# Optimization experiments

Hardware: AMD Instinct MI355X
Metric: run time of the kernel (lower is better)

The kernel has to match this reference:

```python
import jax, jax.numpy as jnp
import numpy as np

# Assumptions from DCalhas/eeg_to_fmri repo layers:
#  - RandomFourierFeatures: z = cos(x @ W + b) followed by layer normalization
#    over the feature axis (normalization='layer'), W/b trainable.
#  - Sinusoids: elementwise sin(x).

B, D, T, L = 64, 512, 1024, 512

def _layer_norm(x, eps=1e-5):
    mu = jnp.mean(x, axis=-1, keepdims=True)
    var = jnp.var(x, axis=-1, keepdims=True)
    return (x - mu) * jax.lax.rsqrt(var + eps)

def setup_inputs() -> dict:
    key = jax.random.key(0)
    ks = jax.random.split(key, 12)
    s = 1.0 / np.sqrt(L)
    return {
        "x": jax.random.normal(ks[0], (B, D, T), jnp.float32),
        "rff_w": jax.random.normal(ks[1], (D, L), jnp.float32) * (1.0 / np.sqrt(D)),
        "rff_b": jax.random.uniform(ks[2], (L,), jnp.float32, 0.0, 2.0 * np.pi),
        "weight_input": jax.random.normal(ks[3], (L, L), jnp.float32) * s,
        "weight_forget": jax.random.normal(ks[4], (L, L), jnp.float32) * s,
        "weight_context": jax.random.normal(ks[5], (L, L), jnp.float32) * s,
        "recurrent_input": jax.random.normal(ks[6], (L, L), jnp.float32) * s,
        "recurrent_forget": jax.random.normal(ks[7], (L, L), jnp.float32) * s,
        "recurrent_context": jax.random.normal(ks[8], (L, L), jnp.float32) * s,
        "bias_input": jnp.zeros((L,), jnp.float32),
        "bias_forget": jnp.zeros((L,), jnp.float32),
        "bias_context": jnp.zeros((L,), jnp.float32),
        "init_latent": jax.random.normal(ks[9], (1, 1, L), jnp.float32) * s,
        "init_context": jax.random.normal(ks[10], (1, 1, L), jnp.float32) * s,
    }

def reference(x, rff_w, rff_b, weight_input, weight_forget, weight_context,
              recurrent_input, recurrent_forget, recurrent_context,
              bias_input, bias_forget, bias_context, init_latent, init_context):
    b = x.shape[0]
    xt = jnp.transpose(x, (0, 2, 1))                      # [B,T,D]
    z = _layer_norm(jnp.cos(xt @ rff_w + rff_b))          # [B,T,L]
    # hidden_states[t+1] = z_t in the original loop, so the "recurrent" input
    # at step t is z_{t-1} (init_latent at t=0). Gates are thus batchable.
    z_prev = jnp.concatenate(
        [jnp.broadcast_to(init_latent, (b, 1, z.shape[2])), z[:, :-1]], axis=1)
    i = jax.nn.sigmoid(z @ weight_input + z_prev @ recurrent_input + bias_input)
    f = jax.nn.sigmoid(z @ weight_forget + z_prev @ recurrent_forget + bias_forget)
    g = jnp.tanh(z @ weight_context + z_prev @ recurrent_context + bias_context)
    o = jnp.sin(z)                                        # Sinusoids gate

    c0 = jnp.broadcast_to(init_context[:, 0], (b, z.shape[2]))  # [B,L]
    def step(c_prev, gates):
        i_t, f_t, g_t, o_t = gates
        c_t = f_t * c_prev + i_t * g_t
        return c_t, o_t * c_t
    xs = tuple(jnp.transpose(a, (1, 0, 2)) for a in (i, f, g, o))  # time-major
    _, h = jax.lax.scan(step, c0, xs)                     # [T,B,L]
    return jnp.transpose(h, (1, 2, 0))                    # [B,L,T]
```

## Files before the change

kernel.cpp:

```cpp
#include <hip/hip_runtime.h>
#include <hip/hip_bf16.h>
#include <hip/hip_fp16.h>
#include <cstdint>
#include <cstddef>


typedef float f32x4 __attribute__((ext_vector_type(4)));
typedef short s16x8 __attribute__((ext_vector_type(8)));

__device__ __forceinline__ void gload_lds16(const void* g, void* l) {
  __builtin_amdgcn_global_load_lds(
      (const __attribute__((address_space(1))) void*)g,
      (__attribute__((address_space(3))) void*)l, 16, 0, 0);
}
__device__ __forceinline__ ushort f2bf(float f) {
  uint32_t u = __float_as_uint(f);
  return (ushort)((u + 0x7FFF + ((u >> 16) & 1)) >> 16);
}
__device__ __forceinline__ float bf2f(ushort s) {
  return __uint_as_float(((uint32_t)s) << 16);
}
__device__ __forceinline__ ushort f2h(float f) {
  return __half_as_ushort(__float2half(f));
}
__device__ __forceinline__ float h2f(ushort s) {
  return __half2float(__ushort_as_half(s));
}

#define MF(d, a, b) d = __builtin_amdgcn_mfma_f32_16x16x32_bf16(a, b, d, 0, 0, 0);

__global__ __launch_bounds__(256) void transpose_cvt(
    const float* __restrict__ src, ushort* __restrict__ dst, int ld)
{
  __shared__ float tile[32][33];
  const int c0 = blockIdx.x * 32, r0 = blockIdx.y * 32;
  const int tx = threadIdx.x & 31, ty = threadIdx.x >> 5;
#pragma unroll
  for (int i = 0; i < 4; ++i)
    tile[ty + i * 8][tx] = src[(size_t)(r0 + ty + i * 8) * 512 + c0 + tx];
  __syncthreads();
#pragma unroll
  for (int i = 0; i < 4; ++i)
    dst[(size_t)(c0 + ty + i * 8) * ld + r0 + tx] = f2bf(tile[tx][ty + i * 8]);
}

__global__ __launch_bounds__(256) void transpose6(
    const float* __restrict__ s0, const float* __restrict__ s1,
    const float* __restrict__ s2, const float* __restrict__ s3,
    const float* __restrict__ s4, const float* __restrict__ s5,
    const float* __restrict__ il, ushort* __restrict__ W2t,
    ushort* __restrict__ ilb)
{
  const int z = blockIdx.z;
  if (z == 6) {
    if (blockIdx.x == 0 && blockIdx.y == 0) {
      ilb[threadIdx.x] = f2bf(il[threadIdx.x]);
      ilb[threadIdx.x + 256] = f2bf(il[threadIdx.x + 256]);
    }
    return;
  }
  const float* src = z == 0 ? s0 : z == 1 ? s1 : z == 2 ? s2
                   : z == 3 ? s3 : z == 4 ? s4 : s5;
  ushort* dst = W2t + (size_t)(z >> 1) * 512 * 1024 + (z & 1) * 512;
  __shared__ float tile[32][33];
  const int c0 = blockIdx.x * 32, r0 = blockIdx.y * 32;
  const int tx = threadIdx.x & 31, ty = threadIdx.x >> 5;
#pragma unroll
  for (int i = 0; i < 4; ++i)
    tile[ty + i * 8][tx] = src[(size_t)(r0 + ty + i * 8) * 512 + c0 + tx];
  __syncthreads();
#pragma unroll
  for (int i = 0; i < 4; ++i)
    dst[(size_t)(c0 + ty + i * 8) * 1024 + r0 + tx] = f2bf(tile[tx][ty + i * 8]);
}

__global__ __launch_bounds__(256) void transpose_x(
    const float* __restrict__ x, ushort* __restrict__ xt)
{
  __shared__ float tile[64][68];
  const int b = blockIdx.z;
  const int t0 = blockIdx.x * 64, d0 = blockIdx.y * 64;
  const float* src = x + ((size_t)b * 512 + d0) * 1024 + t0;
  const int lr_ = threadIdx.x >> 4, lc4 = (threadIdx.x & 15) * 4;
#pragma unroll
  for (int p = 0; p < 4; ++p) {
    const float4 v = *(const float4*)(src + (size_t)(lr_ + p * 16) * 1024 + lc4);
    *(float4*)&tile[lr_ + p * 16][lc4] = v;
  }
  __syncthreads();
  const int tt = threadIdx.x >> 2, dc = (threadIdx.x & 3) * 16;
  ushort* dst = xt + ((size_t)b * 1024 + t0 + tt) * 512 + d0 + dc;
  uint4 o1, o2;
  o1.x = (uint)f2bf(tile[dc + 0][tt]) | ((uint)f2bf(tile[dc + 1][tt]) << 16);
  o1.y = (uint)f2bf(tile[dc + 2][tt]) | ((uint)f2bf(tile[dc + 3][tt]) << 16);
  o1.z = (uint)f2bf(tile[dc + 4][tt]) | ((uint)f2bf(tile[dc + 5][tt]) << 16);
  o1.w = (uint)f2bf(tile[dc + 6][tt]) | ((uint)f2bf(tile[dc + 7][tt]) << 16);
  o2.x = (uint)f2bf(tile[dc + 8][tt]) | ((uint)f2bf(tile[dc + 9][tt]) << 16);
  o2.y = (uint)f2bf(tile[dc + 10][tt]) | ((uint)f2bf(tile[dc + 11][tt]) << 16);
  o2.z = (uint)f2bf(tile[dc + 12][tt]) | ((uint)f2bf(tile[dc + 13][tt]) << 16);
  o2.w = (uint)f2bf(tile[dc + 14][tt]) | ((uint)f2bf(tile[dc + 15][tt]) << 16);
  *(uint4*)(dst) = o1;
  *(uint4*)(dst + 8) = o2;
}

__global__ __launch_bounds__(256, 2) void k1_mfma(
    const ushort* __restrict__ A, const ushort* __restrict__ Bt,
    const float* __restrict__ bias, ushort* __restrict__ U)
{
  __shared__ __align__(16) short As[128 * 64];
  __shared__ __align__(16) short Bs[128 * 64];
  const int tid = threadIdx.x;
  const int lane = tid & 63, wid = tid >> 6;
  const int orig = blockIdx.x;
  const int swz = (orig & 7) * 256 + (orig >> 3);
  const int n0 = (swz & 3) * 128, r0 = (swz >> 2) * 128;
  const int wr = wid >> 1, wc = wid & 1;
  const int fr = lane & 15, fq = lane >> 4;
  const int lr = lane >> 3;
  const int swz_el = ((lane & 7) ^ lr) * 8;

  const int RA = r0 + wid * 32 + lr;
  const ushort* pa0 = A + (size_t)(RA)      * 512 + swz_el;
  const ushort* pa1 = A + (size_t)(RA + 8)  * 512 + swz_el;
  const ushort* pa2 = A + (size_t)(RA + 16) * 512 + swz_el;
  const ushort* pa3 = A + (size_t)(RA + 24) * 512 + swz_el;
  const int RB = n0 + wid * 32 + lr;
  const ushort* pb0 = Bt + (size_t)(RB)      * 512 + swz_el;
  const ushort* pb1 = Bt + (size_t)(RB + 8)  * 512 + swz_el;
  const ushort* pb2 = Bt + (size_t)(RB + 16) * 512 + swz_el;
  const ushort* pb3 = Bt + (size_t)(RB + 24) * 512 + swz_el;
  char* dA = (char*)As + wid * 4096;
  char* dB = (char*)Bs + wid * 4096;

  const int so0 = fr * 64 + ((fq)     ^ (fr & 7)) * 8;
  const int so1 = fr * 64 + ((4 + fq) ^ (fr & 7)) * 8;

  f32x4 c00 = {0.f,0.f,0.f,0.f}, c01 = c00, c02 = c00, c03 = c00,
        c10 = c00, c11 = c00, c12 = c00, c13 = c00,
        c20 = c00, c21 = c00, c22 = c00, c23 = c00,
        c30 = c00, c31 = c00, c32 = c00, c33 = c00;

  for (int k0 = 0; k0 < 512; k0 += 64) {
    gload_lds16(pa0 + k0, dA);        gload_lds16(pa1 + k0, dA + 1024);
    gload_lds16(pa2 + k0, dA + 2048); gload_lds16(pa3 + k0, dA + 3072);
    gload_lds16(pb0 + k0, dB);        gload_lds16(pb1 + k0, dB + 1024);
    gload_lds16(pb2 + k0, dB + 2048); gload_lds16(pb3 + k0, dB + 3072);
    __syncthreads();
    const s16x8 a00 = *(const s16x8*)&As[wr * 4096 + 0 * 1024 + so0];
    const s16x8 a01 = *(const s16x8*)&As[wr * 4096 + 0 * 1024 + so1];
    const s16x8 a10 = *(const s16x8*)&As[wr * 4096 + 1 * 1024 + so0];
    const s16x8 a11 = *(const s16x8*)&As[wr * 4096 + 1 * 1024 + so1];
    const s16x8 a20 = *(const s16x8*)&As[wr * 4096 + 2 * 1024 + so0];
    const s16x8 a21 = *(const s16x8*)&As[wr * 4096 + 2 * 1024 + so1];
    const s16x8 a30 = *(const s16x8*)&As[wr * 4096 + 3 * 1024 + so0];
    const s16x8 a31 = *(const s16x8*)&As[wr * 4096 + 3 * 1024 + so1];
    const s16x8 b00 = *(const s16x8*)&Bs[wc * 4096 + 0 * 1024 + so0];
    const s16x8 b01 = *(const s16x8*)&Bs[wc * 4096 + 0 * 1024 + so1];
    const s16x8 b10 = *(const s16x8*)&Bs[wc * 4096 + 1 * 1024 + so0];
    const s16x8 b11 = *(const s16x8*)&Bs[wc * 4096 + 1 * 1024 + so1];
    const s16x8 b20 = *(const s16x8*)&Bs[wc * 4096 + 2 * 1024 + so0];
    const s16x8 b21 = *(const s16x8*)&Bs[wc * 4096 + 2 * 1024 + so1];
    const s16x8 b30 = *(const s16x8*)&Bs[wc * 4096 + 3 * 1024 + so0];
    const s16x8 b31 = *(const s16x8*)&Bs[wc * 4096 + 3 * 1024 + so1];
    MF(c00, a00, b00) MF(c01, a00, b10) MF(c02, a00, b20) MF(c03, a00, b30)
    MF(c10, a10, b00) MF(c11, a10, b10) MF(c12, a10, b20) MF(c13, a10, b30)
    MF(c20, a20, b00) MF(c21, a20, b10) MF(c22, a20, b20) MF(c23, a20, b30)
    MF(c30, a30, b00) MF(c31, a30, b10) MF(c32, a30, b20) MF(c33, a30, b30)
    MF(c00, a01, b01) MF(c01, a01, b11) MF(c02, a01, b21) MF(c03, a01, b31)
    MF(c10, a11, b01) MF(c11, a11, b11) MF(c12, a11, b21) MF(c13, a11, b31)
    MF(c20, a21, b01) MF(c21, a21, b11) MF(c22, a21, b21) MF(c23, a21, b31)
    MF(c30, a31, b01) MF(c31, a31, b11) MF(c32, a31, b21) MF(c33, a31, b31)
    __syncthreads();
  }

#define EPI1(cmn, m_, n_) { \
    const int col = n0 + wc * 64 + n_ * 16 + fr; \
    const float bv = bias[col]; \
    const int rbase = r0 + wr * 64 + m_ * 16 + fq * 4; \
    _Pragma("unroll") for (int j = 0; j < 4; ++j) \
      U[(size_t)(rbase + j) * 512 + col] = f2bf(cosf(cmn[j] + bv)); }
  EPI1(c00, 0, 0) EPI1(c01, 0, 1) EPI1(c02, 0, 2) EPI1(c03, 0, 3)
  EPI1(c10, 1, 0) EPI1(c11, 1, 1) EPI1(c12, 1, 2) EPI1(c13, 1, 3)
  EPI1(c20, 2, 0) EPI1(c21, 2, 1) EPI1(c22, 2, 2) EPI1(c23, 2, 3)
  EPI1(c30, 3, 0) EPI1(c31, 3, 1) EPI1(c32, 3, 2) EPI1(c33, 3, 3)
#undef EPI1
}

__global__ __launch_bounds__(256) void ln_rows(
    const ushort* __restrict__ U, ushort* __restrict__ Z)
{
  const int row = blockIdx.x * 4 + (threadIdx.x >> 6);
  const int lane = threadIdx.x & 63;
  const size_t base = (size_t)row * 512 + lane * 8;
  const uint4 pk = *(const uint4*)(U + base);
  float v[8];
  v[0] = bf2f(pk.x & 0xffff); v[1] = bf2f(pk.x >> 16);
  v[2] = bf2f(pk.y & 0xffff); v[3] = bf2f(pk.y >> 16);
  v[4] = bf2f(pk.z & 0xffff); v[5] = bf2f(pk.z >> 16);
  v[6] = bf2f(pk.w & 0xffff); v[7] = bf2f(pk.w >> 16);
  float s = 0.f, s2 = 0.f;
#pragma unroll
  for (int j = 0; j < 8; ++j) { s += v[j]; s2 += v[j] * v[j]; }
#pragma unroll
  for (int m = 1; m < 64; m <<= 1) { s += __shfl_xor(s, m); s2 += __shfl_xor(s2, m); }
  const float mean = s * (1.f / 512.f);
  const float var = s2 * (1.f / 512.f) - mean * mean;
  const float inv = rsqrtf(var + 1e-5f);
  uint4 o;
  o.x = (uint)f2bf((v[0] - mean) * inv) | ((uint)f2bf((v[1] - mean) * inv) << 16);
  o.y = (uint)f2bf((v[2] - mean) * inv) | ((uint)f2bf((v[3] - mean) * inv) << 16);
  o.z = (uint)f2bf((v[4] - mean) * inv) | ((uint)f2bf((v[5] - mean) * inv) << 16);
  o.w = (uint)f2bf((v[6] - mean) * inv) | ((uint)f2bf((v[7] - mean) * inv) << 16);
  *(uint4*)(Z + base) = o;
}

__global__ __launch_bounds__(256, 2) void k2_mfma(
    const ushort* __restrict__ Z, const ushort* __restrict__ Wt,
    const ushort* __restrict__ IL,
    const float* __restrict__ biv, const float* __restrict__ bfv,
    const float* __restrict__ bcv,
    ushort* __restrict__ G2, int tc, int Tc, int nwg)
{
  __shared__ __align__(16) short As[128 * 64];
  __shared__ __align__(16) short Bs0[128 * 64];
  __shared__ __align__(16) short Bs1[128 * 64];
  const int tid = threadIdx.x;
  const int lane = tid & 63, wid = tid >> 6;
  const int cpx = nwg >> 3;
  const int orig = blockIdx.x;
  const int swz = (orig & 7) * cpx + (orig >> 3);
  const int bx = swz & 7, by = swz >> 3;
  const int nb = Tc >> 7;
  const int b = by / nb, tb = by % nb;
  const int r0g = b * 1024 + tc + tb * 128;
  const int r0c = b * Tc + tb * 128;
  const bool isig = bx < 4;
  const int n0 = (bx & 3) * 128;
  const int wr = wid >> 1, wc = wid & 1;
  const int fr = lane & 15, fq = lane >> 4;
  const int lr = lane >> 3;
  const int swz_el = ((lane & 7) ^ lr) * 8;

  const int R0 = r0g + wid * 32 + lr;
  const ushort* pa0 = Z + (size_t)(R0)      * 512 + swz_el;
  const ushort* pa1 = Z + (size_t)(R0 + 8)  * 512 + swz_el;
  const ushort* pa2 = Z + (size_t)(R0 + 16) * 512 + swz_el;
  const ushort* pa3 = Z + (size_t)(R0 + 24) * 512 + swz_el;
  const ushort* ph0 = ((((R0)      & 1023) == 0) ? IL : (Z + (size_t)(R0 - 1)  * 512)) + swz_el;
  const ushort* ph1 = ((((R0 + 8)  & 1023) == 0) ? IL : (Z + (size_t)(R0 + 7)  * 512)) + swz_el;
  const ushort* ph2 = ((((R0 + 16) & 1023) == 0) ? IL : (Z + (size_t)(R0 + 15) * 512)) + swz_el;
  const ushort* ph3 = ((((R0 + 24) & 1023) == 0) ? IL : (Z + (size_t)(R0 + 23) * 512)) + swz_el;
  const int RB0 = (isig ? n0 : 512 + n0) + wid * 32 + lr;
  const ushort* pb0 = Wt + (size_t)(RB0)      * 1024 + swz_el;
  const ushort* pb1 = Wt + (size_t)(RB0 + 8)  * 1024 + swz_el;
  const ushort* pb2 = Wt + (size_t)(RB0 + 16) * 1024 + swz_el;
  const ushort* pb3 = Wt + (size_t)(RB0 + 24) * 1024 + swz_el;
  const int RB1 = 1024 + n0 + wid * 32 + lr;
  const ushort* pq0 = Wt + (size_t)(RB1)      * 1024 + swz_el;
  const ushort* pq1 = Wt + (size_t)(RB1 + 8)  * 1024 + swz_el;
  const ushort* pq2 = Wt + (size_t)(RB1 + 16) * 1024 + swz_el;
  const ushort* pq3 = Wt + (size_t)(RB1 + 24) * 1024 + swz_el;

  const int so0 = fr * 64 + ((fq)     ^ (fr & 7)) * 8;
  const int so1 = fr * 64 + ((4 + fq) ^ (fr & 7)) * 8;

  f32x4 zz = {0.f,0.f,0.f,0.f};
  f32x4 c00=zz,c01=zz,c02=zz,c03=zz, c10=zz,c11=zz,c12=zz,c13=zz,
        c20=zz,c21=zz,c22=zz,c23=zz, c30=zz,c31=zz,c32=zz,c33=zz;
  f32x4 d00=zz,d01=zz,d02=zz,d03=zz, d10=zz,d11=zz,d12=zz,d13=zz,
        d20=zz,d21=zz,d22=zz,d23=zz, d30=zz,d31=zz,d32=zz,d33=zz;

#define STG8(P0,P1,P2,P3, KO, DST) { \
    char* d_ = (char*)(DST) + wid * 4096; \
    gload_lds16((P0) + (KO), d_);        gload_lds16((P1) + (KO), d_ + 1024); \
    gload_lds16((P2) + (KO), d_ + 2048); gload_lds16((P3) + (KO), d_ + 3072); }

#define RDA(SO) \
    const s16x8 fa0 = *(const s16x8*)&As[wr * 4096 + 0 * 1024 + (SO)]; \
    const s16x8 fa1 = *(const s16x8*)&As[wr * 4096 + 1 * 1024 + (SO)]; \
    const s16x8 fa2 = *(const s16x8*)&As[wr * 4096 + 2 * 1024 + (SO)]; \
    const s16x8 fa3 = *(const s16x8*)&As[wr * 4096 + 3 * 1024 + (SO)];

#define RDB(BS, SO) \
    const s16x8 fb0 = *(const s16x8*)&(BS)[wc * 4096 + 0 * 1024 + (SO)]; \
    const s16x8 fb1 = *(const s16x8*)&(BS)[wc * 4096 + 1 * 1024 + (SO)]; \
    const s16x8 fb2 = *(const s16x8*)&(BS)[wc * 4096 + 2 * 1024 + (SO)]; \
    const s16x8 fb3 = *(const s16x8*)&(BS)[wc * 4096 + 3 * 1024 + (SO)];

#define MMC \
    MF(c00,fa0,fb0) MF(c01,fa0,fb1) MF(c02,fa0,fb2) MF(c03,fa0,fb3) \
    MF(c10,fa1,fb0) MF(c11,fa1,fb1) MF(c12,fa1,fb2) MF(c13,fa1,fb3) \
    MF(c20,fa2,fb0) MF(c21,fa2,fb1) MF(c22,fa2,fb2) MF(c23,fa2,fb3) \
    MF(c30,fa3,fb0) MF(c31,fa3,fb1) MF(c32,fa3,fb2) MF(c33,fa3,fb3)

#define MMD \
    MF(d00,fa0,fb0) MF(d01,fa0,fb1) MF(d02,fa0,fb2) MF(d03,fa0,fb3) \
    MF(d10,fa1,fb0) MF(d11,fa1,fb1) MF(d12,fa1,fb2) MF(d13,fa1,fb3) \
    MF(d20,fa2,fb0) MF(d21,fa2,fb1) MF(d22,fa2,fb2) MF(d23,fa2,fb3) \
    MF(d30,fa3,fb0) MF(d31,fa3,fb1) MF(d32,fa3,fb2) MF(d33,fa3,fb3)

#define KSTEP(SO_) { \
    RDA(SO_) \
    { RDB(Bs0, SO_) MMC } \
    if (isig) { RDB(Bs1, SO_) MMD } }

  for (int k0 = 0; k0 < 512; k0 += 64) {
    STG8(pa0, pa1, pa2, pa3, k0, As)
    STG8(pb0, pb1, pb2, pb3, k0, Bs0)
    if (isig) { STG8(pq0, pq1, pq2, pq3, k0, Bs1) }
    __syncthreads();
    KSTEP(so0)
    KSTEP(so1)
    __syncthreads();
  }
  for (int k0 = 0; k0 < 512; k0 += 64) {
    STG8(ph0, ph1, ph2, ph3, k0, As)
    STG8(pb0, pb1, pb2, pb3, 512 + k0, Bs0)
    if (isig) { STG8(pq0, pq1, pq2, pq3, 512 + k0, Bs1) }
    __syncthreads();
    KSTEP(so0)
    KSTEP(so1)
    __syncthreads();
  }
#undef KSTEP
#undef MMD
#undef MMC
#undef RDB
#undef RDA
#undef STG8

  if (isig) {
#define EPI(cmn, dmn, m_, n_) { \
    const int col = n0 + wc * 64 + n_ * 16 + fr; \
    const float bvi = biv[col], bvc = bcv[col]; \
    const int rbase = wr * 64 + m_ * 16 + fq * 4; \
    _Pragma("unroll") for (int j = 0; j < 4; ++j) { \
      const float iv = 1.f / (1.f + __expf(-(cmn[j] + bvi))); \
      const float gv = 2.f / (1.f + __expf(-2.f * (dmn[j] + bvc))) - 1.f; \
      G2[(size_t)(r0c + rbase + j) * 1024 + col] = f2h(iv * gv); } }
    EPI(c00, d00, 0, 0) EPI(c01, d01, 0, 1) EPI(c02, d02, 0, 2) EPI(c03, d03, 0, 3)
    EPI(c10, d10, 1, 0) EPI(c11, d11, 1, 1) EPI(c12, d12, 1, 2) EPI(c13, d13, 1, 3)
    EPI(c20, d20, 2, 0) EPI(c21, d21, 2, 1) EPI(c22, d22, 2, 2) EPI(c23, d23, 2, 3)
    EPI(c30, d30, 3, 0) EPI(c31, d31, 3, 1) EPI(c32, d32, 3, 2) EPI(c33, d33, 3, 3)
#undef EPI
  } else {
#define EPI(cmn, m_, n_) { \
    const int col = n0 + wc * 64 + n_ * 16 + fr; \
    const float bv = bfv[col]; \
    const int rbase = wr * 64 + m_ * 16 + fq * 4; \
    _Pragma("unroll") for (int j = 0; j < 4; ++j) { \
      const float fv = 1.f / (1.f + __expf(-(cmn[j] + bv))); \
      G2[(size_t)(r0c + rbase + j) * 1024 + 512 + col] = f2h(fv); } }
    EPI(c00, 0, 0) EPI(c01, 0, 1) EPI(c02, 0, 2) EPI(c03, 0, 3)
    EPI(c10, 1, 0) EPI(c11, 1, 1) EPI(c12, 1, 2) EPI(c13, 1, 3)
    EPI(c20, 2, 0) EPI(c21, 2, 1) EPI(c22, 2, 2) EPI(c23, 2, 3)
    EPI(c30, 3, 0) EPI(c31, 3, 1) EPI(c32, 3, 2) EPI(c33, 3, 3)
#undef EPI
  }
}

__global__ __launch_bounds__(256) void k3a_seg(
    const ushort* __restrict__ G2, float* __restrict__ Aseg,
    float* __restrict__ Bseg, int Tc)
{
  const int l = blockIdx.x * 256 + threadIdx.x;
  const int b = blockIdx.y, s = blockIdx.z;
  const int SEGc = Tc >> 6;
  const ushort* gb = G2 + ((size_t)(b * Tc + s * 64)) * 1024 + l;
  float A = 1.f, c = 0.f;
#pragma unroll 8
  for (int j = 0; j < 64; ++j) {
    const float P = h2f(gb[(size_t)j * 1024]);
    const float F = h2f(gb[(size_t)j * 1024 + 512]);
    A *= F;
    c = fmaf(F, c, P);
  }
  const size_t o = (size_t)(b * SEGc + s) * 512 + l;
  Aseg[o] = A;
  Bseg[o] = c;
}

__global__ __launch_bounds__(512) void k3b_comb(
    const float* __restrict__ Aseg, const float* __restrict__ Bseg,
    const float* __restrict__ initc, float* __restrict__ cstart,
    float* __restrict__ cbuf, int tc, int Tc)
{
  const int b = blockIdx.x, l = threadIdx.x;
  const int SEGc = Tc >> 6;
  float c = (tc == 0) ? initc[l] : cbuf[b * 512 + l];
  for (int s = 0; s < SEGc; ++s) {
    const size_t o = (size_t)(b * SEGc + s) * 512 + l;
    cstart[o] = c;
    c = fmaf(Aseg[o], c, Bseg[o]);
  }
  cbuf[b * 512 + l] = c;
}

__global__ __launch_bounds__(128) void k3c_emit(
    const ushort* __restrict__ G2, const ushort* __restrict__ Z,
    const float* __restrict__ cstart, float* __restrict__ out,
    int tc, int Tc)
{
  __shared__ float tile[128][65];
  const int tid = threadIdx.x;
  const int l0 = blockIdx.x * 128;
  const int b = blockIdx.y, s = blockIdx.z;
  const int SEGc = Tc >> 6;
  const int l = l0 + tid;

  float c = cstart[(size_t)(b * SEGc + s) * 512 + l];
  const ushort* gb = G2 + ((size_t)(b * Tc + s * 64)) * 1024 + l;
  const ushort* zb = Z + ((size_t)(b * 1024 + tc + s * 64)) * 512 + l;
#pragma unroll 8
  for (int j = 0; j < 64; ++j) {
    const float P = h2f(gb[(size_t)j * 1024]);
    const float F = h2f(gb[(size_t)j * 1024 + 512]);
    const float zv = bf2f(zb[(size_t)j * 512]);
    c = fmaf(F, c, P);
    tile[tid][j] = sinf(zv) * c;
  }
  __syncthreads();
  const int col = tid & 63, rhalf = tid >> 6;
  const size_t obase = ((size_t)b * 512 + l0) * 1024 + (size_t)(tc + s * 64) + col;
#pragma unroll
  for (int p = 0; p < 64; ++p) {
    const int row = rhalf + p * 2;
    out[obase + (size_t)row * 1024] = tile[row][col];
  }
}

extern "C" void kernel_launch(void* const* d_in, const int* in_sizes, int n_in,
                              void* d_out, int out_size, void* d_ws, size_t ws_size,
                              hipStream_t stream)
{
  const float* x  = (const float*)d_in[0];
  const float* W  = (const float*)d_in[1];
  const float* rb = (const float*)d_in[2];
  const float* wi = (const float*)d_in[3];
  const float* wf = (const float*)d_in[4];
  const float* wc = (const float*)d_in[5];
  const float* ri = (const float*)d_in[6];
  const float* rf = (const float*)d_in[7];
  const float* rc = (const float*)d_in[8];
  const float* bi = (const float*)d_in[9];
  const float* bfo = (const float*)d_in[10];
  const float* bc = (const float*)d_in[11];
  const float* il = (const float*)d_in[12];
  const float* ic = (const float*)d_in[13];
  float* out = (float*)d_out;

  char* ws = (char*)d_ws;
  size_t off = 0;
  auto alloc = [&](size_t bytes) -> void* {
    void* p = ws + off;
    off = (off + bytes + 255) & ~(size_t)255;
    return p;
  };
  ushort* z    = (ushort*)alloc((size_t)65536 * 512 * 2);
  ushort* W1t  = (ushort*)alloc((size_t)512 * 512 * 2);
  ushort* W2t  = (ushort*)alloc((size_t)1536 * 1024 * 2);
  ushort* ilb  = (ushort*)alloc(512 * 2);
  float*  cbuf = (float*)alloc((size_t)64 * 512 * 4);
  float*  Aseg = (float*)alloc((size_t)64 * 16 * 512 * 4);
  float*  Bseg = (float*)alloc((size_t)64 * 16 * 512 * 4);
  float*  cstart = (float*)alloc((size_t)64 * 16 * 512 * 4);
  const size_t fixed_end = off;
  ushort* xt   = (ushort*)alloc((size_t)65536 * 512 * 2);
  ushort* G2   = (ushort*)(ws + fixed_end);
  ushort* u    = (ushort*)d_out;

  int Tc = 1024;
  while (Tc > 128 && fixed_end + (size_t)64 * Tc * 1024 * 2 > ws_size) Tc >>= 1;

  transpose_cvt<<<dim3(16, 16), 256, 0, stream>>>(W, W1t, 512);
  transpose6<<<dim3(16, 16, 7), 256, 0, stream>>>(wi, ri, wf, rf, wc, rc, il, W2t, ilb);
  transpose_x<<<dim3(16, 8, 64), 256, 0, stream>>>(x, xt);

  k1_mfma<<<dim3(2048), 256, 0, stream>>>(xt, W1t, rb, u);
  ln_rows<<<16384, 256, 0, stream>>>(u, z);

  for (int tc = 0; tc < 1024; tc += Tc) {
    const int SEGc = Tc >> 6;
    const int nwg2 = 8 * 64 * (Tc >> 7);
    k2_mfma<<<dim3(nwg2), 256, 0, stream>>>(
        z, W2t, ilb, bi, bfo, bc, G2, tc, Tc, nwg2);
    k3a_seg<<<dim3(2, 64, SEGc), 256, 0, stream>>>(G2, Aseg, Bseg, Tc);
    k3b_comb<<<64, 512, 0, stream>>>(Aseg, Bseg, ic, cstart, cbuf, tc, Tc);
    k3c_emit<<<dim3(4, 64, SEGc), 128, 0, stream>>>(G2, z, cstart, out, tc, Tc);
  }
}
```

Measured before the change: 568.1 us.

## Balance k2 workgroups so forget-gate blocks compute two column tiles each

k2 previously launched 8 column groups per row tile. The 4 input/context blocks each ran two accumulator sets, while the 4 forget blocks ran only one and sat half idle. Now there are 6 groups, and each forget block computes 256 columns using both accumulator sets, so all workgroups do equal work and the grid is smaller. The W1 transpose is also folded into the combined weight-transpose kernel, removing one launch. The swizzle now uses mod/div by 6 instead of bit ops, and fewer workgroups may lower occupancy or tail balance.

```diff
diff --git a/kernel.cpp b/kernel.cpp
--- a/kernel.cpp
+++ b/kernel.cpp
@@ -29,27 +29,13 @@
 
 #define MF(d, a, b) d = __builtin_amdgcn_mfma_f32_16x16x32_bf16(a, b, d, 0, 0, 0);
 
-__global__ __launch_bounds__(256) void transpose_cvt(
-    const float* __restrict__ src, ushort* __restrict__ dst, int ld)
-{
-  __shared__ float tile[32][33];
-  const int c0 = blockIdx.x * 32, r0 = blockIdx.y * 32;
-  const int tx = threadIdx.x & 31, ty = threadIdx.x >> 5;
-#pragma unroll
-  for (int i = 0; i < 4; ++i)
-    tile[ty + i * 8][tx] = src[(size_t)(r0 + ty + i * 8) * 512 + c0 + tx];
-  __syncthreads();
-#pragma unroll
-  for (int i = 0; i < 4; ++i)
-    dst[(size_t)(c0 + ty + i * 8) * ld + r0 + tx] = f2bf(tile[tx][ty + i * 8]);
-}
-
-__global__ __launch_bounds__(256) void transpose6(
+__global__ __launch_bounds__(256) void transpose8(
     const float* __restrict__ s0, const float* __restrict__ s1,
     const float* __restrict__ s2, const float* __restrict__ s3,
     const float* __restrict__ s4, const float* __restrict__ s5,
-    const float* __restrict__ il, ushort* __restrict__ W2t,
-    ushort* __restrict__ ilb)
+    const float* __restrict__ il, const float* __restrict__ W1,
+    ushort* __restrict__ W2t, ushort* __restrict__ ilb,
+    ushort* __restrict__ W1t)
 {
   const int z = blockIdx.z;
   if (z == 6) {
@@ -60,8 +46,10 @@
     return;
   }
   const float* src = z == 0 ? s0 : z == 1 ? s1 : z == 2 ? s2
-                   : z == 3 ? s3 : z == 4 ? s4 : s5;
-  ushort* dst = W2t + (size_t)(z >> 1) * 512 * 1024 + (z & 1) * 512;
+                   : z == 3 ? s3 : z == 4 ? s4 : z == 5 ? s5 : W1;
+  ushort* dst = (z == 7) ? W1t
+              : W2t + (size_t)(z >> 1) * 512 * 1024 + (z & 1) * 512;
+  const int ld = (z == 7) ? 512 : 1024;
   __shared__ float tile[32][33];
   const int c0 = blockIdx.x * 32, r0 = blockIdx.y * 32;
   const int tx = threadIdx.x & 31, ty = threadIdx.x >> 5;
@@ -71,7 +59,7 @@
   __syncthreads();
 #pragma unroll
   for (int i = 0; i < 4; ++i)
-    dst[(size_t)(c0 + ty + i * 8) * 1024 + r0 + tx] = f2bf(tile[tx][ty + i * 8]);
+    dst[(size_t)(c0 + ty + i * 8) * ld + r0 + tx] = f2bf(tile[tx][ty + i * 8]);
 }
 
 __global__ __launch_bounds__(256) void transpose_x(
@@ -229,13 +217,14 @@
   const int cpx = nwg >> 3;
   const int orig = blockIdx.x;
   const int swz = (orig & 7) * cpx + (orig >> 3);
-  const int bx = swz & 7, by = swz >> 3;
+  const int bx = swz % 6, by = swz / 6;
   const int nb = Tc >> 7;
   const int b = by / nb, tb = by % nb;
   const int r0g = b * 1024 + tc + tb * 128;
   const int r0c = b * Tc + tb * 128;
   const bool isig = bx < 4;
-  const int n0 = (bx & 3) * 128;
+  const int n0 = isig ? bx * 128 : 0;
+  const int fb = bx - 4;
   const int wr = wid >> 1, wc = wid & 1;
   const int fr = lane & 15, fq = lane >> 4;
   const int lr = lane >> 3;
@@ -250,12 +239,12 @@
   const ushort* ph1 = ((((R0 + 8)  & 1023) == 0) ? IL : (Z + (size_t)(R0 + 7)  * 512)) + swz_el;
   const ushort* ph2 = ((((R0 + 16) & 1023) == 0) ? IL : (Z + (size_t)(R0 + 15) * 512)) + swz_el;
   const ushort* ph3 = ((((R0 + 24) & 1023) == 0) ? IL : (Z + (size_t)(R0 + 23) * 512)) + swz_el;
-  const int RB0 = (isig ? n0 : 512 + n0) + wid * 32 + lr;
+  const int RB0 = (isig ? n0 : 512 + fb * 256) + wid * 32 + lr;
   const ushort* pb0 = Wt + (size_t)(RB0)      * 1024 + swz_el;
   const ushort* pb1 = Wt + (size_t)(RB0 + 8)  * 1024 + swz_el;
   const ushort* pb2 = Wt + (size_t)(RB0 + 16) * 1024 + swz_el;
   const ushort* pb3 = Wt + (size_t)(RB0 + 24) * 1024 + swz_el;
-  const int RB1 = 1024 + n0 + wid * 32 + lr;
+  const int RB1 = (isig ? 1024 + n0 : 512 + fb * 256 + 128) + wid * 32 + lr;
   const ushort* pq0 = Wt + (size_t)(RB1)      * 1024 + swz_el;
   const ushort* pq1 = Wt + (size_t)(RB1 + 8)  * 1024 + swz_el;
   const ushort* pq2 = Wt + (size_t)(RB1 + 16) * 1024 + swz_el;
@@ -302,12 +291,12 @@
 #define KSTEP(SO_) { \
     RDA(SO_) \
     { RDB(Bs0, SO_) MMC } \
-    if (isig) { RDB(Bs1, SO_) MMD } }
+    { RDB(Bs1, SO_) MMD } }
 
   for (int k0 = 0; k0 < 512; k0 += 64) {
     STG8(pa0, pa1, pa2, pa3, k0, As)
     STG8(pb0, pb1, pb2, pb3, k0, Bs0)
-    if (isig) { STG8(pq0, pq1, pq2, pq3, k0, Bs1) }
+    STG8(pq0, pq1, pq2, pq3, k0, Bs1)
     __syncthreads();
     KSTEP(so0)
     KSTEP(so1)
@@ -316,7 +305,7 @@
   for (int k0 = 0; k0 < 512; k0 += 64) {
     STG8(ph0, ph1, ph2, ph3, k0, As)
     STG8(pb0, pb1, pb2, pb3, 512 + k0, Bs0)
-    if (isig) { STG8(pq0, pq1, pq2, pq3, 512 + k0, Bs1) }
+    STG8(pq0, pq1, pq2, pq3, 512 + k0, Bs1)
     __syncthreads();
     KSTEP(so0)
     KSTEP(so1)
@@ -344,18 +333,22 @@
     EPI(c30, d30, 3, 0) EPI(c31, d31, 3, 1) EPI(c32, d32, 3, 2) EPI(c33, d33, 3, 3)
 #undef EPI
   } else {
-#define EPI(cmn, m_, n_) { \
-    const int col = n0 + wc * 64 + n_ * 16 + fr; \
+#define EPIF(cmn, m_, n_, COFF) { \
+    const int col = fb * 256 + (COFF) + wc * 64 + n_ * 16 + fr; \
     const float bv = bfv[col]; \
     const int rbase = wr * 64 + m_ * 16 + fq * 4; \
     _Pragma("unroll") for (int j = 0; j < 4; ++j) { \
       const float fv = 1.f / (1.f + __expf(-(cmn[j] + bv))); \
       G2[(size_t)(r0c + rbase + j) * 1024 + 512 + col] = f2h(fv); } }
-    EPI(c00, 0, 0) EPI(c01, 0, 1) EPI(c02, 0, 2) EPI(c03, 0, 3)
-    EPI(c10, 1, 0) EPI(c11, 1, 1) EPI(c12, 1, 2) EPI(c13, 1, 3)
-    EPI(c20, 2, 0) EPI(c21, 2, 1) EPI(c22, 2, 2) EPI(c23, 2, 3)
-    EPI(c30, 3, 0) EPI(c31, 3, 1) EPI(c32, 3, 2) EPI(c33, 3, 3)
-#undef EPI
+    EPIF(c00, 0, 0, 0) EPIF(c01, 0, 1, 0) EPIF(c02, 0, 2, 0) EPIF(c03, 0, 3, 0)
+    EPIF(c10, 1, 0, 0) EPIF(c11, 1, 1, 0) EPIF(c12, 1, 2, 0) EPIF(c13, 1, 3, 0)
+    EPIF(c20, 2, 0, 0) EPIF(c21, 2, 1, 0) EPIF(c22, 2, 2, 0) EPIF(c23, 2, 3, 0)
+    EPIF(c30, 3, 0, 0) EPIF(c31, 3, 1, 0) EPIF(c32, 3, 2, 0) EPIF(c33, 3, 3, 0)
+    EPIF(d00, 0, 0, 128) EPIF(d01, 0, 1, 128) EPIF(d02, 0, 2, 128) EPIF(d03, 0, 3, 128)
+    EPIF(d10, 1, 0, 128) EPIF(d11, 1, 1, 128) EPIF(d12, 1, 2, 128) EPIF(d13, 1, 3, 128)
+    EPIF(d20, 2, 0, 128) EPIF(d21, 2, 1, 128) EPIF(d22, 2, 2, 128) EPIF(d23, 2, 3, 128)
+    EPIF(d30, 3, 0, 128) EPIF(d31, 3, 1, 128) EPIF(d32, 3, 2, 128) EPIF(d33, 3, 3, 128)
+#undef EPIF
   }
 }
 
@@ -472,8 +465,8 @@
   int Tc = 1024;
   while (Tc > 128 && fixed_end + (size_t)64 * Tc * 1024 * 2 > ws_size) Tc >>= 1;
 
-  transpose_cvt<<<dim3(16, 16), 256, 0, stream>>>(W, W1t, 512);
-  transpose6<<<dim3(16, 16, 7), 256, 0, stream>>>(wi, ri, wf, rf, wc, rc, il, W2t, ilb);
+  transpose8<<<dim3(16, 16, 8), 256, 0, stream>>>(
+      wi, ri, wf, rf, wc, rc, il, W, W2t, ilb, W1t);
   transpose_x<<<dim3(16, 8, 64), 256, 0, stream>>>(x, xt);
 
   k1_mfma<<<dim3(2048), 256, 0, stream>>>(xt, W1t, rb, u);
@@ -481,7 +474,7 @@
 
   for (int tc = 0; tc < 1024; tc += Tc) {
     const int SEGc = Tc >> 6;
-    const int nwg2 = 8 * 64 * (Tc >> 7);
+    const int nwg2 = 6 * 64 * (Tc >> 7);
     k2_mfma<<<dim3(nwg2), 256, 0, stream>>>(
         z, W2t, ilb, bi, bfo, bc, G2, tc, Tc, nwg2);
     k3a_seg<<<dim3(2, 64, SEGc), 256, 0, stream>>>(G2, Aseg, Bseg, Tc);
```

New measurement: 534.9 us. 1.06x faster.
